# Kernel optimization log

Measured on AMD Instinct MI355X. Metric: run time of the kernel, lower is better.

## Reference

```python
import jax, jax.numpy as jnp
import numpy as np

B = 16384      # batch
IN = 512       # input width
G, F, O = 64, 24, 16      # hidden: groups, fan_in, group_out (width = G*O = 1024)
GO_G, GO_F, GO_O = 4, 48, 16  # output layer: 4 groups x 16 = 64 outputs


def setup_inputs() -> dict:
    key = jax.random.key(0)
    ks = jax.random.split(key, 13)
    # total columns available (concat of input + all prior hidden layers)
    tot = [IN, IN + G * O, IN + 2 * G * O, IN + 3 * G * O]  # 512,1536,2560,3584
    scale = 0.1
    return {
        "x": jax.random.normal(ks[0], (B, IN), jnp.float32),
        "W1": jax.random.normal(ks[1], (G, F, O), jnp.float32) * scale,
        "b1": jnp.zeros((G, O), jnp.float32),
        "W2": jax.random.normal(ks[2], (G, F, O), jnp.float32) * scale,
        "b2": jnp.zeros((G, O), jnp.float32),
        "W3": jax.random.normal(ks[3], (G, F, O), jnp.float32) * scale,
        "b3": jnp.zeros((G, O), jnp.float32),
        "Wo": jax.random.normal(ks[4], (GO_G, GO_F, GO_O), jnp.float32) * scale,
        "bo": jnp.zeros((GO_G, GO_O), jnp.float32),
        "idx1": jax.random.randint(ks[5], (G, F), 0, tot[0], jnp.int32),
        "idx2": jax.random.randint(ks[6], (G, F), 0, tot[1], jnp.int32),
        "idx3": jax.random.randint(ks[7], (G, F), 0, tot[2], jnp.int32),
        "idxo": jax.random.randint(ks[8], (GO_G, GO_F), 0, tot[3], jnp.int32),
    }


def _group_layer(acc, idx, W, b, act):
    # acc: [B, P] concat of all prior layer outputs; idx: [G, F] column coords
    g = acc[:, idx]                               # [B, G, F] irregular gather
    h = jnp.einsum('bgf,gfo->bgo', g, W) + b      # many tiny dense sublayers
    h = act(h)
    return h.reshape(h.shape[0], -1)              # concat groups -> [B, G*O]


def reference(x, W1, b1, W2, b2, W3, b3, Wo, bo, idx1, idx2, idx3, idxo):
    acc = x
    for idx, W, b in ((idx1, W1, b1), (idx2, W2, b2), (idx3, W3, b3)):
        out = _group_layer(acc, idx, W, b, jnp.tanh)
        acc = jnp.concatenate([acc, out], axis=1)  # inputs.append(layer_out)
    # output layer uses linear out_activation
    return _group_layer(acc, idxo, Wo, bo, lambda h: h)  # [B, 64]
```

## Files before the change

kernel.cpp:

```cpp
#include <hip/hip_runtime.h>
#include <hip/hip_bf16.h>


typedef unsigned short ushort_t;
typedef unsigned int uint_t;
typedef __attribute__((ext_vector_type(8))) short short8;
typedef __attribute__((ext_vector_type(4))) float f32x4;

#define ACC_STRIDE 3588
#define ROW_BYTES (ACC_STRIDE * 2)
#define PAD_ONE 3584
#define ONE_BYTE (PAD_ONE * 2)
#define ZERO_BYTE (3586 * 2)
#define ACC_U16 (16 * ACC_STRIDE)
#define OFFS_BYTES 25600
#define LDS_BYTES (ACC_U16 * 2 + OFFS_BYTES)

#define OFF_HID_B 204800
#define OFF_HEAD_B 229376

__device__ __forceinline__ ushort_t f2bf(float f) {
    __hip_bfloat16 h = __float2bfloat16(f);
    union { __hip_bfloat16 h; ushort_t u; } v;
    v.h = h;
    return v.u;
}

__device__ __forceinline__ uint_t pack2bf(float lo, float hi) {
    return (uint_t)f2bf(lo) | ((uint_t)f2bf(hi) << 16);
}

__device__ __forceinline__ float fast_tanh(float x) {
    float e = __expf(2.0f * x);
    return fmaf(-2.0f, __builtin_amdgcn_rcpf(e + 1.0f), 1.0f);
}

__global__ __launch_bounds__(256)
void convert_weights(const float* __restrict__ W1, const float* __restrict__ b1,
                     const float* __restrict__ W2, const float* __restrict__ b2,
                     const float* __restrict__ W3, const float* __restrict__ b3,
                     const float* __restrict__ Wo, const float* __restrict__ bo,
                     const int* __restrict__ idx1, const int* __restrict__ idx2,
                     const int* __restrict__ idx3, const int* __restrict__ idxo,
                     ushort_t* __restrict__ ws)
{
    const int tid = blockIdx.x * 256 + threadIdx.x;
    const int lane = tid & 63;
    const int nn = lane & 15;
    const int quad = lane >> 4;
    if (tid < 12288) {
        const int g = (tid >> 6) & 63;
        const int l = tid >> 12;
        const float* W = (l == 0) ? W1 : (l == 1) ? W2 : W3;
        const float* bb = (l == 0) ? b1 : (l == 1) ? b2 : b3;
        const float* Wg = W + g * 384;
        ushort_t v[8];
        #pragma unroll
        for (int j = 0; j < 8; ++j) {
            const int k = quad * 8 + j;
            v[j] = (k < 24) ? f2bf(Wg[k * 16 + nn])
                 : (k == 24) ? f2bf(bb[g * 16 + nn]) : (ushort_t)0;
        }
        ushort4* dst = reinterpret_cast<ushort4*>(ws + (size_t)tid * 8);
        dst[0] = make_ushort4(v[0], v[1], v[2], v[3]);
        dst[1] = make_ushort4(v[4], v[5], v[6], v[7]);
    } else if (tid < 12800) {
        const int h = tid - 12288;
        const int gs = h >> 6;
        const int go = gs >> 1;
        const int step = gs & 1;
        const float* Wg = Wo + go * 768;
        ushort_t v[8];
        #pragma unroll
        for (int j = 0; j < 8; ++j) {
            const int k = step * 32 + quad * 8 + j;
            v[j] = (k < 48) ? f2bf(Wg[k * 16 + nn])
                 : (k == 48) ? f2bf(bo[go * 16 + nn]) : (ushort_t)0;
        }
        ushort4* dst = reinterpret_cast<ushort4*>(ws + (size_t)tid * 8);
        dst[0] = make_ushort4(v[0], v[1], v[2], v[3]);
        dst[1] = make_ushort4(v[4], v[5], v[6], v[7]);
    } else if (tid < 18944) {
        const int e = tid - 12800;
        const int l = e >> 11;
        const int rem = e & 2047;
        const int g = rem >> 5;
        const int k = rem & 31;
        const int* idx = (l == 0) ? idx1 : (l == 1) ? idx2 : idx3;
        const int v = (k < 24) ? idx[g * 24 + k] * 2
                    : (k == 24) ? ONE_BYTE : ZERO_BYTE;
        reinterpret_cast<int*>((char*)ws + OFF_HID_B)[e] = v;
    } else if (tid < 19200) {
        const int e = tid - 18944;
        const int go = e >> 6;
        const int k = e & 63;
        const int v = (k < 48) ? idxo[go * 48 + k] * 2
                    : (k == 48) ? ONE_BYTE : ZERO_BYTE;
        reinterpret_cast<int*>((char*)ws + OFF_HEAD_B)[e] = v;
    }
}

#define NTILES 4

__global__ __launch_bounds__(1024)
void demodel_mfma(const float* __restrict__ x,
                  const ushort_t* __restrict__ ws,
                  float* __restrict__ out)
{
    extern __shared__ __align__(16) ushort_t smem[];
    const int t = threadIdx.x;
    const int lane = t & 63;
    const int wv = t >> 6;
    const int nn = lane & 15;
    const int quad = lane >> 4;

    {
        const uint4* src = reinterpret_cast<const uint4*>((const char*)ws + OFF_HID_B);
        uint4* dst = reinterpret_cast<uint4*>(smem + ACC_U16);
        for (int i = t; i < OFFS_BYTES / 16; i += 1024)
            dst[i] = src[i];
    }
    if (t < 16) {
        uint2* p = reinterpret_cast<uint2*>((char*)smem + t * ROW_BYTES + ONE_BYTE);
        *p = make_uint2(0x00003f80u, 0u);
    }

    const int* offs = reinterpret_cast<const int*>(smem + ACC_U16);
    const char* accb = (const char*)smem + nn * ROW_BYTES;
    char* accw = (char*)smem;

    const int pr = (t - 512) >> 5;
    const int pc = (t & 31) << 4;
    uint_t px[8];

    if (wv >= 8) {
        const float4* src = reinterpret_cast<const float4*>(
            x + ((size_t)blockIdx.x * 16 + pr) * 512 + pc);
        float4 a0 = src[0], a1 = src[1], a2 = src[2], a3 = src[3];
        px[0] = pack2bf(a0.x, a0.y); px[1] = pack2bf(a0.z, a0.w);
        px[2] = pack2bf(a1.x, a1.y); px[3] = pack2bf(a1.z, a1.w);
        px[4] = pack2bf(a2.x, a2.y); px[5] = pack2bf(a2.z, a2.w);
        px[6] = pack2bf(a3.x, a3.y); px[7] = pack2bf(a3.z, a3.w);
    }

    #pragma unroll 1
    for (int it = 0; it < NTILES; ++it) {
        const int row0 = (it * 256 + blockIdx.x) * 16;

        __syncthreads();
        if (wv >= 8) {
            uint2* d = reinterpret_cast<uint2*>(accw + pr * ROW_BYTES + pc * 2);
            d[0] = make_uint2(px[0], px[1]);
            d[1] = make_uint2(px[2], px[3]);
            d[2] = make_uint2(px[4], px[5]);
            d[3] = make_uint2(px[6], px[7]);
        }
        __syncthreads();

        #pragma unroll 1
        for (int l = 0; l < 3; ++l) {
            const int out_base = 512 + l * 1024;
            const int g0 = wv << 2;

            int4 o0[4], o1[4];
            short8 bfr[4];
            #pragma unroll
            for (int gi = 0; gi < 4; ++gi) {
                const int* op = offs + l * 2048 + (g0 + gi) * 32 + quad * 8;
                o0[gi] = *reinterpret_cast<const int4*>(op);
                o1[gi] = *reinterpret_cast<const int4*>(op + 4);
                bfr[gi] = *reinterpret_cast<const short8*>(
                    ws + (((size_t)l * 64 + g0 + gi) * 64 + lane) * 8);
            }

            short8 af[4];
            #pragma unroll
            for (int gi = 0; gi < 4; ++gi) {
                af[gi][0] = *(const short*)(accb + o0[gi].x);
                af[gi][1] = *(const short*)(accb + o0[gi].y);
                af[gi][2] = *(const short*)(accb + o0[gi].z);
                af[gi][3] = *(const short*)(accb + o0[gi].w);
                af[gi][4] = *(const short*)(accb + o1[gi].x);
                af[gi][5] = *(const short*)(accb + o1[gi].y);
                af[gi][6] = *(const short*)(accb + o1[gi].z);
                af[gi][7] = *(const short*)(accb + o1[gi].w);
            }

            f32x4 acc[4];
            #pragma unroll
            for (int gi = 0; gi < 4; ++gi) {
                f32x4 z = { 0.f, 0.f, 0.f, 0.f };
                acc[gi] = __builtin_amdgcn_mfma_f32_16x16x32_bf16(bfr[gi], af[gi], z, 0, 0, 0);
            }

            #pragma unroll
            for (int gi = 0; gi < 4; ++gi) {
                uint2 q;
                q.x = pack2bf(fast_tanh(acc[gi][0]), fast_tanh(acc[gi][1]));
                q.y = pack2bf(fast_tanh(acc[gi][2]), fast_tanh(acc[gi][3]));
                *reinterpret_cast<uint2*>(
                    (char*)smem + nn * ROW_BYTES +
                    (out_base + (g0 + gi) * 16 + quad * 4) * 2) = q;
            }
            __syncthreads();
        }

        if (wv < 4) {
            const int go = wv;
            int4 o0[2], o1[2];
            short8 bfr[2];
            #pragma unroll
            for (int s = 0; s < 2; ++s) {
                const int* op = offs + 6144 + go * 64 + s * 32 + quad * 8;
                o0[s] = *reinterpret_cast<const int4*>(op);
                o1[s] = *reinterpret_cast<const int4*>(op + 4);
                bfr[s] = *reinterpret_cast<const short8*>(
                    ws + (12288 + ((size_t)go * 2 + s) * 64 + lane) * 8);
            }
            short8 af[2];
            #pragma unroll
            for (int s = 0; s < 2; ++s) {
                af[s][0] = *(const short*)(accb + o0[s].x);
                af[s][1] = *(const short*)(accb + o0[s].y);
                af[s][2] = *(const short*)(accb + o0[s].z);
                af[s][3] = *(const short*)(accb + o0[s].w);
                af[s][4] = *(const short*)(accb + o1[s].x);
                af[s][5] = *(const short*)(accb + o1[s].y);
                af[s][6] = *(const short*)(accb + o1[s].z);
                af[s][7] = *(const short*)(accb + o1[s].w);
            }
            f32x4 z = { 0.f, 0.f, 0.f, 0.f };
            f32x4 a0 = __builtin_amdgcn_mfma_f32_16x16x32_bf16(bfr[0], af[0], z, 0, 0, 0);
            f32x4 a1 = __builtin_amdgcn_mfma_f32_16x16x32_bf16(bfr[1], af[1], z, 0, 0, 0);
            float4 v = make_float4(a0[0] + a1[0], a0[1] + a1[1],
                                   a0[2] + a1[2], a0[3] + a1[3]);
            *reinterpret_cast<float4*>(
                out + (size_t)(row0 + nn) * 64 + go * 16 + quad * 4) = v;
        }
        if (wv >= 8 && it + 1 < NTILES) {
            const float4* src = reinterpret_cast<const float4*>(
                x + (((size_t)(it + 1) * 256 + blockIdx.x) * 16 + pr) * 512 + pc);
            float4 a0 = src[0], a1 = src[1], a2 = src[2], a3 = src[3];
            px[0] = pack2bf(a0.x, a0.y); px[1] = pack2bf(a0.z, a0.w);
            px[2] = pack2bf(a1.x, a1.y); px[3] = pack2bf(a1.z, a1.w);
            px[4] = pack2bf(a2.x, a2.y); px[5] = pack2bf(a2.z, a2.w);
            px[6] = pack2bf(a3.x, a3.y); px[7] = pack2bf(a3.z, a3.w);
        }
    }
}

extern "C" void kernel_launch(void* const* d_in, const int* in_sizes, int n_in,
                              void* d_out, int out_size, void* d_ws, size_t ws_size,
                              hipStream_t stream) {
    const float* x  = (const float*)d_in[0];
    const float* W1 = (const float*)d_in[1];
    const float* b1 = (const float*)d_in[2];
    const float* W2 = (const float*)d_in[3];
    const float* b2 = (const float*)d_in[4];
    const float* W3 = (const float*)d_in[5];
    const float* b3 = (const float*)d_in[6];
    const float* Wo = (const float*)d_in[7];
    const float* bo = (const float*)d_in[8];
    const int* idx1 = (const int*)d_in[9];
    const int* idx2 = (const int*)d_in[10];
    const int* idx3 = (const int*)d_in[11];
    const int* idxo = (const int*)d_in[12];
    float* out = (float*)d_out;

    (void)hipFuncSetAttribute((const void*)demodel_mfma,
                              hipFuncAttributeMaxDynamicSharedMemorySize,
                              LDS_BYTES);

    convert_weights<<<75, 256, 0, stream>>>(W1, b1, W2, b2, W3, b3, Wo, bo,
                                            idx1, idx2, idx3, idxo,
                                            (ushort_t*)d_ws);

    demodel_mfma<<<256, 1024, LDS_BYTES, stream>>>(
        x, (const ushort_t*)d_ws, out);
}
```

Before: 122.1 us.

## Pack gather offsets as 16-bit, keep them in registers, gather layer-1 from global

Gather offset tables are shrunk from 32-bit to 16-bit entries, loaded from LDS once per block and held in registers for all tiles and layers, so the per-layer LDS offset loads go away. Layer 1 now gathers its inputs directly from global x (as float, converted to bf16 in registers) and builds the bias lane in registers, instead of reading the staged bf16 copy in LDS. The layer loop is unrolled and B-fragment loads are moved next to their MFMA. The cost is higher register pressure and scattered, uncoalesced global loads for layer 1.

```diff
diff --git a/kernel.cpp b/kernel.cpp
--- a/kernel.cpp
+++ b/kernel.cpp
@@ -13,11 +13,10 @@
 #define ONE_BYTE (PAD_ONE * 2)
 #define ZERO_BYTE (3586 * 2)
 #define ACC_U16 (16 * ACC_STRIDE)
-#define OFFS_BYTES 25600
-#define LDS_BYTES (ACC_U16 * 2 + OFFS_BYTES)
-
-#define OFF_HID_B 204800
-#define OFF_HEAD_B 229376
+#define TBL_BYTES 12800
+#define LDS_BYTES (ACC_U16 * 2 + TBL_BYTES)
+
+#define OFF_B 204800
 
 __device__ __forceinline__ ushort_t f2bf(float f) {
     __hip_bfloat16 h = __float2bfloat16(f);
@@ -83,20 +82,24 @@
     } else if (tid < 18944) {
         const int e = tid - 12800;
         const int l = e >> 11;
-        const int rem = e & 2047;
-        const int g = rem >> 5;
-        const int k = rem & 31;
-        const int* idx = (l == 0) ? idx1 : (l == 1) ? idx2 : idx3;
-        const int v = (k < 24) ? idx[g * 24 + k] * 2
-                    : (k == 24) ? ONE_BYTE : ZERO_BYTE;
-        reinterpret_cast<int*>((char*)ws + OFF_HID_B)[e] = v;
+        const int g = (e >> 5) & 63;
+        const int k = e & 31;
+        ushort_t v;
+        if (l == 0) {
+            v = (k < 24) ? (ushort_t)idx1[g * 24 + k] : (ushort_t)0;
+        } else {
+            const int* idx = (l == 1) ? idx2 : idx3;
+            v = (k < 24) ? (ushort_t)(idx[g * 24 + k] * 2)
+              : (k == 24) ? (ushort_t)ONE_BYTE : (ushort_t)ZERO_BYTE;
+        }
+        reinterpret_cast<ushort_t*>((char*)ws + OFF_B)[e] = v;
     } else if (tid < 19200) {
         const int e = tid - 18944;
         const int go = e >> 6;
         const int k = e & 63;
-        const int v = (k < 48) ? idxo[go * 48 + k] * 2
-                    : (k == 48) ? ONE_BYTE : ZERO_BYTE;
-        reinterpret_cast<int*>((char*)ws + OFF_HEAD_B)[e] = v;
+        const ushort_t v = (k < 48) ? (ushort_t)(idxo[go * 48 + k] * 2)
+                         : (k == 48) ? (ushort_t)ONE_BYTE : (ushort_t)ZERO_BYTE;
+        reinterpret_cast<ushort_t*>((char*)ws + OFF_B)[6144 + e] = v;
     }
 }
 
@@ -113,26 +116,37 @@
     const int wv = t >> 6;
     const int nn = lane & 15;
     const int quad = lane >> 4;
-
-    {
-        const uint4* src = reinterpret_cast<const uint4*>((const char*)ws + OFF_HID_B);
-        uint4* dst = reinterpret_cast<uint4*>(smem + ACC_U16);
-        for (int i = t; i < OFFS_BYTES / 16; i += 1024)
-            dst[i] = src[i];
-    }
+    const bool q3 = (quad == 3);
+
+    if (t < TBL_BYTES / 16)
+        reinterpret_cast<uint4*>(smem + ACC_U16)[t] =
+            reinterpret_cast<const uint4*>((const char*)ws + OFF_B)[t];
     if (t < 16) {
         uint2* p = reinterpret_cast<uint2*>((char*)smem + t * ROW_BYTES + ONE_BYTE);
         *p = make_uint2(0x00003f80u, 0u);
     }
-
-    const int* offs = reinterpret_cast<const int*>(smem + ACC_U16);
+    __syncthreads();
+
+    const ushort_t* tbl = smem + ACC_U16;
+    uint4 ofh[3][4];
+    #pragma unroll
+    for (int l = 0; l < 3; ++l)
+        #pragma unroll
+        for (int gi = 0; gi < 4; ++gi)
+            ofh[l][gi] = *reinterpret_cast<const uint4*>(
+                tbl + (l << 11) + (((wv << 2) + gi) << 5) + (quad << 3));
+    uint4 ofo[2];
+    if (wv < 4) {
+        ofo[0] = *reinterpret_cast<const uint4*>(tbl + 6144 + (wv << 6) + (quad << 3));
+        ofo[1] = *reinterpret_cast<const uint4*>(tbl + 6144 + (wv << 6) + 32 + (quad << 3));
+    }
+
     const char* accb = (const char*)smem + nn * ROW_BYTES;
     char* accw = (char*)smem;
 
     const int pr = (t - 512) >> 5;
     const int pc = (t & 31) << 4;
     uint_t px[8];
-
     if (wv >= 8) {
         const float4* src = reinterpret_cast<const float4*>(
             x + ((size_t)blockIdx.x * 16 + pr) * 512 + pc);
@@ -147,6 +161,17 @@
     for (int it = 0; it < NTILES; ++it) {
         const int row0 = (it * 256 + blockIdx.x) * 16;
 
+        const float* xrow = x + (size_t)(row0 + nn) * 512;
+        float f0[4][8];
+        #pragma unroll
+        for (int gi = 0; gi < 4; ++gi) {
+            const uint4 o = ofh[0][gi];
+            f0[gi][0] = xrow[o.x & 0xFFFFu]; f0[gi][1] = xrow[o.x >> 16];
+            f0[gi][2] = xrow[o.y & 0xFFFFu]; f0[gi][3] = xrow[o.y >> 16];
+            f0[gi][4] = xrow[o.z & 0xFFFFu]; f0[gi][5] = xrow[o.z >> 16];
+            f0[gi][6] = xrow[o.w & 0xFFFFu]; f0[gi][7] = xrow[o.w >> 16];
+        }
+
         __syncthreads();
         if (wv >= 8) {
             uint2* d = reinterpret_cast<uint2*>(accw + pr * ROW_BYTES + pc * 2);
@@ -157,47 +182,55 @@
         }
         __syncthreads();
 
-        #pragma unroll 1
-        for (int l = 0; l < 3; ++l) {
+        {
+            const int g0 = wv << 2;
+            #pragma unroll
+            for (int gi = 0; gi < 4; ++gi) {
+                short8 af;
+                af[0] = q3 ? (short)0x3f80 : (short)f2bf(f0[gi][0]);
+                #pragma unroll
+                for (int j = 1; j < 8; ++j)
+                    af[j] = q3 ? (short)0 : (short)f2bf(f0[gi][j]);
+                const short8 bfr = *reinterpret_cast<const short8*>(
+                    ws + ((size_t)(g0 + gi) * 64 + lane) * 8);
+                f32x4 z = { 0.f, 0.f, 0.f, 0.f };
+                f32x4 acc = __builtin_amdgcn_mfma_f32_16x16x32_bf16(bfr, af, z, 0, 0, 0);
+                uint2 q;
+                q.x = pack2bf(fast_tanh(acc[0]), fast_tanh(acc[1]));
+                q.y = pack2bf(fast_tanh(acc[2]), fast_tanh(acc[3]));
+                *reinterpret_cast<uint2*>(
+                    (char*)smem + nn * ROW_BYTES +
+                    (512 + (g0 + gi) * 16 + quad * 4) * 2) = q;
+            }
+            __syncthreads();
+        }
+
+        #pragma unroll
+        for (int l = 1; l < 3; ++l) {
             const int out_base = 512 + l * 1024;
             const int g0 = wv << 2;
-
-            int4 o0[4], o1[4];
-            short8 bfr[4];
-            #pragma unroll
-            for (int gi = 0; gi < 4; ++gi) {
-                const int* op = offs + l * 2048 + (g0 + gi) * 32 + quad * 8;
-                o0[gi] = *reinterpret_cast<const int4*>(op);
-                o1[gi] = *reinterpret_cast<const int4*>(op + 4);
-                bfr[gi] = *reinterpret_cast<const short8*>(
-                    ws + (((size_t)l * 64 + g0 + gi) * 64 + lane) * 8);
-            }
-
             short8 af[4];
             #pragma unroll
             for (int gi = 0; gi < 4; ++gi) {
-                af[gi][0] = *(const short*)(accb + o0[gi].x);
-                af[gi][1] = *(const short*)(accb + o0[gi].y);
-                af[gi][2] = *(const short*)(accb + o0[gi].z);
-                af[gi][3] = *(const short*)(accb + o0[gi].w);
-                af[gi][4] = *(const short*)(accb + o1[gi].x);
-                af[gi][5] = *(const short*)(accb + o1[gi].y);
-                af[gi][6] = *(const short*)(accb + o1[gi].z);
-                af[gi][7] = *(const short*)(accb + o1[gi].w);
+                const uint4 o = ofh[l][gi];
+                af[gi][0] = *(const short*)(accb + (o.x & 0xFFFFu));
+                af[gi][1] = *(const short*)(accb + (o.x >> 16));
+                af[gi][2] = *(const short*)(accb + (o.y & 0xFFFFu));
+                af[gi][3] = *(const short*)(accb + (o.y >> 16));
+                af[gi][4] = *(const short*)(accb + (o.z & 0xFFFFu));
+                af[gi][5] = *(const short*)(accb + (o.z >> 16));
+                af[gi][6] = *(const short*)(accb + (o.w & 0xFFFFu));
+                af[gi][7] = *(const short*)(accb + (o.w >> 16));
             }
-
-            f32x4 acc[4];
             #pragma unroll
             for (int gi = 0; gi < 4; ++gi) {
+                const short8 bfr = *reinterpret_cast<const short8*>(
+                    ws + (((size_t)l * 64 + g0 + gi) * 64 + lane) * 8);
                 f32x4 z = { 0.f, 0.f, 0.f, 0.f };
-                acc[gi] = __builtin_amdgcn_mfma_f32_16x16x32_bf16(bfr[gi], af[gi], z, 0, 0, 0);
-            }
-
-            #pragma unroll
-            for (int gi = 0; gi < 4; ++gi) {
+                f32x4 acc = __builtin_amdgcn_mfma_f32_16x16x32_bf16(bfr, af[gi], z, 0, 0, 0);
                 uint2 q;
-                q.x = pack2bf(fast_tanh(acc[gi][0]), fast_tanh(acc[gi][1]));
-                q.y = pack2bf(fast_tanh(acc[gi][2]), fast_tanh(acc[gi][3]));
+                q.x = pack2bf(fast_tanh(acc[0]), fast_tanh(acc[1]));
+                q.y = pack2bf(fast_tanh(acc[2]), fast_tanh(acc[3]));
                 *reinterpret_cast<uint2*>(
                     (char*)smem + nn * ROW_BYTES +
                     (out_base + (g0 + gi) * 16 + quad * 4) * 2) = q;
@@ -207,31 +240,26 @@
 
         if (wv < 4) {
             const int go = wv;
-            int4 o0[2], o1[2];
-            short8 bfr[2];
-            #pragma unroll
-            for (int s = 0; s < 2; ++s) {
-                const int* op = offs + 6144 + go * 64 + s * 32 + quad * 8;
-                o0[s] = *reinterpret_cast<const int4*>(op);
-                o1[s] = *reinterpret_cast<const int4*>(op + 4);
-                bfr[s] = *reinterpret_cast<const short8*>(
-                    ws + (12288 + ((size_t)go * 2 + s) * 64 + lane) * 8);
-            }
             short8 af[2];
             #pragma unroll
             for (int s = 0; s < 2; ++s) {
-                af[s][0] = *(const short*)(accb + o0[s].x);
-                af[s][1] = *(const short*)(accb + o0[s].y);
-                af[s][2] = *(const short*)(accb + o0[s].z);
-                af[s][3] = *(const short*)(accb + o0[s].w);
-                af[s][4] = *(const short*)(accb + o1[s].x);
-                af[s][5] = *(const short*)(accb + o1[s].y);
-                af[s][6] = *(const short*)(accb + o1[s].z);
-                af[s][7] = *(const short*)(accb + o1[s].w);
+                const uint4 o = ofo[s];
+                af[s][0] = *(const short*)(accb + (o.x & 0xFFFFu));
+                af[s][1] = *(const short*)(accb + (o.x >> 16));
+                af[s][2] = *(const short*)(accb + (o.y & 0xFFFFu));
+                af[s][3] = *(const short*)(accb + (o.y >> 16));
+                af[s][4] = *(const short*)(accb + (o.z & 0xFFFFu));
+                af[s][5] = *(const short*)(accb + (o.z >> 16));
+                af[s][6] = *(const short*)(accb + (o.w & 0xFFFFu));
+                af[s][7] = *(const short*)(accb + (o.w >> 16));
             }
+            const short8 bf0 = *reinterpret_cast<const short8*>(
+                ws + (12288 + ((size_t)go * 2 + 0) * 64 + lane) * 8);
+            const short8 bf1 = *reinterpret_cast<const short8*>(
+                ws + (12288 + ((size_t)go * 2 + 1) * 64 + lane) * 8);
             f32x4 z = { 0.f, 0.f, 0.f, 0.f };
-            f32x4 a0 = __builtin_amdgcn_mfma_f32_16x16x32_bf16(bfr[0], af[0], z, 0, 0, 0);
-            f32x4 a1 = __builtin_amdgcn_mfma_f32_16x16x32_bf16(bfr[1], af[1], z, 0, 0, 0);
+            f32x4 a0 = __builtin_amdgcn_mfma_f32_16x16x32_bf16(bf0, af[0], z, 0, 0, 0);
+            f32x4 a1 = __builtin_amdgcn_mfma_f32_16x16x32_bf16(bf1, af[1], z, 0, 0, 0);
             float4 v = make_float4(a0[0] + a1[0], a0[1] + a1[1],
                                    a0[2] + a1[2], a0[3] + a1[3]);
             *reinterpret_cast<float4*>(
```

Result: slower. 236.5 us (+93.7%).
